# Kernel optimization log

Hardware: AMD Instinct MI355X
Metric: run time of the kernel (lower is better)

Reference implementation:

```python
import jax, jax.numpy as jnp
import numpy as np

B, S, HID = 1, 2048, 4096
NH, NKV, HD = 32, 8, 128
EPS = 1e-6
SCALE = HD ** -0.5


def _rope_cos_sin(seq_len, head_dim, base=1000000.0):
    inv_freq = 1.0 / (base ** (np.arange(0, head_dim, 2, dtype=np.float32) / head_dim))
    t = np.arange(seq_len, dtype=np.float32)
    freqs = np.outer(t, inv_freq)                      # [S, HD/2]
    emb = np.concatenate([freqs, freqs], axis=-1)       # [S, HD]
    return jnp.asarray(np.cos(emb))[None], jnp.asarray(np.sin(emb))[None]  # [1,S,HD]


def setup_inputs() -> dict:
    key = jax.random.key(0)
    ks = jax.random.split(key, 8)
    cos, sin = _rope_cos_sin(S, HD)
    inp = {
        "hidden_states": jax.random.normal(ks[0], (B, S, HID), jnp.float32),
        "cos": jnp.broadcast_to(cos, (B, S, HD)),
        "sin": jnp.broadcast_to(sin, (B, S, HD)),
        "Wq": jax.random.normal(ks[1], (NH * HD, HID), jnp.float32) * 0.02,
        "Wk": jax.random.normal(ks[2], (NKV * HD, HID), jnp.float32) * 0.02,
        "Wv": jax.random.normal(ks[3], (NKV * HD, HID), jnp.float32) * 0.02,
        "Wo": jax.random.normal(ks[4], (HID, NH * HD), jnp.float32) * 0.02,
        "q_norm_w": jnp.ones((HD,), jnp.float32),
        "k_norm_w": jnp.ones((HD,), jnp.float32),
    }
    return inp


def _rmsnorm(x, w, eps=EPS):
    var = jnp.mean(jnp.square(x), axis=-1, keepdims=True)
    return x * jax.lax.rsqrt(var + eps) * w


def _rotate_half(x):
    x1, x2 = jnp.split(x, 2, axis=-1)
    return jnp.concatenate([-x2, x1], axis=-1)


def _apply_rope(x, cos, sin):
    # x: [b,s,n,d]; cos/sin: [b,s,d] -> unsqueeze head dim (dim=2)
    c = cos[:, :, None, :]
    s = sin[:, :, None, :]
    return x * c + _rotate_half(x) * s


def reference(hidden_states, cos, sin, Wq, Wk, Wv, Wo, q_norm_w, k_norm_w):
    b, s, _ = hidden_states.shape
    q = (hidden_states @ Wq.T).reshape(b, s, NH, HD)
    k = (hidden_states @ Wk.T).reshape(b, s, NKV, HD)
    v = (hidden_states @ Wv.T).reshape(b, s, NKV, HD)
    # per-head RMSNorm on q and k
    q = _rmsnorm(q, q_norm_w)
    k = _rmsnorm(k, k_norm_w)
    # RoPE
    q = _apply_rope(q, cos, sin)
    k = _apply_rope(k, cos, sin)
    # GQA: expand kv heads to match query heads (group size = NH // NKV)
    g = NH // NKV
    k = jnp.repeat(k, g, axis=2)  # [b,s,NH,d]
    v = jnp.repeat(v, g, axis=2)
    # causal SDPA, layout bsnd
    scores = jnp.einsum("bqhd,bkhd->bhqk", q, k) * SCALE
    causal = jnp.tril(jnp.ones((s, s), dtype=bool))
    scores = jnp.where(causal[None, None], scores, jnp.finfo(scores.dtype).min)
    probs = jax.nn.softmax(scores, axis=-1)
    attn = jnp.einsum("bhqk,bkhd->bqhd", probs, v).reshape(b, s, NH * HD)
    return attn @ Wo.T
```

## Files before the change

kernel.cpp:

```cpp
#include <hip/hip_runtime.h>
#include <hip/hip_bf16.h>
#include <stdint.h>

#define S_LEN 2048
#define HIDD  4096
#define NH    32
#define NKV   8
#define HD    128
#define NQKV  6144
#define ATT_SCALE 0.08838834764831845f
#define LOG2E 1.4426950408889634f

typedef unsigned short u16;
typedef __attribute__((ext_vector_type(8))) short short8;
typedef __attribute__((ext_vector_type(4))) float f32x4;

__device__ __forceinline__ unsigned f2bfbits(float f){
  union{float f; unsigned u;} v; v.f = f;
  return (v.u + 0x7FFFu + ((v.u>>16)&1u)) >> 16;
}
__device__ __forceinline__ float bf2f(u16 b){
  union{unsigned u; float f;} v; v.u = ((unsigned)b)<<16;
  return v.f;
}
__device__ __forceinline__ unsigned packbf(float a, float b){
  return f2bfbits(a) | (f2bfbits(b)<<16);
}
__device__ __forceinline__ unsigned cvtpk(float lo, float hi){
  unsigned r;
  asm("v_cvt_pk_bf16_f32 %0, %1, %2" : "=v"(r) : "v"(lo), "v"(hi));
  return r;
}

#define GLOAD16(g, l) __builtin_amdgcn_global_load_lds( \
    (__attribute__((address_space(1))) void*)(g), \
    (__attribute__((address_space(3))) void*)(l), 16, 0, 0)

#define VMWAIT(n) asm volatile("s_waitcnt vmcnt(" #n ")" ::: "memory")
#define SCHED0() __builtin_amdgcn_sched_barrier(0)

__global__ __launch_bounds__(256) void cvt_all(const float* __restrict__ hs,
                                               const float* __restrict__ Wq,
                                               const float* __restrict__ Wk,
                                               const float* __restrict__ Wv,
                                               u16* __restrict__ Xb,
                                               u16* __restrict__ WQKV){
  const float* src; u16* dst; int n8;
  switch (blockIdx.y){
    case 0: src = hs; dst = Xb;                        n8 = S_LEN*HIDD/8;    break;
    case 1: src = Wq; dst = WQKV;                      n8 = NH*HD*HIDD/8;    break;
    case 2: src = Wk; dst = WQKV + (size_t)NH*HD*HIDD; n8 = NKV*HD*HIDD/8;   break;
    default:src = Wv; dst = WQKV + (size_t)(NH+NKV)*HD*HIDD; n8 = NKV*HD*HIDD/8; break;
  }
  int i = blockIdx.x*256 + threadIdx.x;
  if (i >= n8) return;
  const float4* p = (const float4*)src;
  float4 a = p[2*i], b = p[2*i+1];
  union { unsigned u[4]; short8 s; } o;
  o.u[0] = packbf(a.x, a.y); o.u[1] = packbf(a.z, a.w);
  o.u[2] = packbf(b.x, b.y); o.u[3] = packbf(b.z, b.w);
  *(short8*)(dst + (size_t)i*8) = o.s;
}

__global__ __launch_bounds__(256) void cvt_bf16(const float* __restrict__ in,
                                                u16* __restrict__ out, int n8){
  int i = blockIdx.x*256 + threadIdx.x;
  if (i >= n8) return;
  const float4* p = (const float4*)in;
  float4 a = p[2*i], b = p[2*i+1];
  union { unsigned u[4]; short8 s; } o;
  o.u[0] = packbf(a.x, a.y); o.u[1] = packbf(a.z, a.w);
  o.u[2] = packbf(b.x, b.y); o.u[3] = packbf(b.z, b.w);
  *(short8*)(out + (size_t)i*8) = o.s;
}

template<int BM, int BN, typename OT>
__global__ __launch_bounds__(256) void gemm_4ph(const u16* __restrict__ A,
                                                const u16* __restrict__ B,
                                                OT* __restrict__ C,
                                                int N, int K, int nbx){
  constexpr int MREP = BM/32;
  constexpr int NF   = BN/32;
  constexpr int AL   = BM/64;
  constexpr int BL   = BN/64;
  constexpr int ASZ  = BM*64;
  constexpr int BSZ  = BN*64;
  __shared__ __align__(16) char lds[4*ASZ + 4*BSZ];

  const int tid = threadIdx.x;
  const int w = tid>>6, lane = tid&63, ln = lane&15, g = lane>>4;
  const int wm = w>>1, wn = w&1;
  const int swz5 = ((ln>>3)&1)<<5;

  const int nwg = gridDim.x, flat = blockIdx.x;
  const int wg = (flat&7)*(nwg>>3) + (flat>>3);
  const int by = wg/nbx, bx = wg - by*nbx;
  const int m0 = by*BM, n0 = bx*BN;

  const int rs   = ((tid>>6)<<4) + ((tid&63)>>2);
  const int ksrc = ((tid&3)<<3) ^ (((tid>>5)&1)<<4);
  const u16* srcA[AL];
  #pragma unroll
  for (int j=0;j<AL;j++) srcA[j] = A + (size_t)(m0 + 64*j + rs)*K + ksrc;
  const u16* srcB[BL];
  #pragma unroll
  for (int j=0;j<BL;j++) srcB[j] = B + (size_t)(n0 + 64*j + rs)*K + ksrc;

  #define AREG(bf,kh) (lds + ((bf)*2 + (kh))*ASZ)
  #define BREG(bf,kh) (lds + 4*ASZ + ((bf)*2 + (kh))*BSZ)

  #define STAGEPT(t, kh, bf) { const int off_ = (t)*64 + (kh)*32;                 \
    _Pragma("unroll") for (int j=0;j<AL;j++)                                      \
      GLOAD16(srcA[j]+off_, AREG(bf,kh) + (4*j+w)*1024);                          \
    _Pragma("unroll") for (int j=0;j<BL;j++)                                      \
      GLOAD16(srcB[j]+off_, BREG(bf,kh) + (4*j+w)*1024); }

  f32x4 acc[MREP][NF];
  #pragma unroll
  for (int m=0;m<MREP;m++)
    #pragma unroll
    for (int n=0;n<NF;n++) acc[m][n] = (f32x4){0.f,0.f,0.f,0.f};
  short8 a_[MREP], b_[NF];

  #define READA(bf,kh) { _Pragma("unroll") for (int m=0;m<MREP;m++)               \
    a_[m] = *(const short8*)(AREG(bf,kh) + (wm*MREP+m)*1024 + ln*64 + ((g*16)^swz5)); }
  #define READB(bf,kh) { _Pragma("unroll") for (int n=0;n<NF;n++)                 \
    b_[n] = *(const short8*)(BREG(bf,kh) + (wn*NF+n)*1024 + ln*64 + ((g*16)^swz5)); }
  #define MFMACLU() { __builtin_amdgcn_s_setprio(1);                              \
    _Pragma("unroll") for (int m=0;m<MREP;m++)                                    \
      _Pragma("unroll") for (int n=0;n<NF;n++)                                    \
        acc[m][n] = __builtin_amdgcn_mfma_f32_16x16x32_bf16(a_[m], b_[n], acc[m][n], 0,0,0); \
    __builtin_amdgcn_s_setprio(0); }
  #define BARR() __builtin_amdgcn_s_barrier()
  #define VM2LP() do{ if constexpr (AL+BL==5) { VMWAIT(10); } else { VMWAIT(8); } }while(0)
  #define VM1LP() do{ if constexpr (AL+BL==5) { VMWAIT(5); }  else { VMWAIT(4); } }while(0)

  STAGEPT(0,0,0); STAGEPT(0,1,0); STAGEPT(1,0,1);
  VMWAIT(0); BARR(); SCHED0();

  const int NIT = K>>7;
  #pragma unroll 1
  for (int it=0; it<NIT; ++it){
    const bool last = (it == NIT-1);
    const int t0 = 2*it;
    READB(0,0); READA(0,0); STAGEPT(t0+1, 1, 1);
    MFMACLU();
    SCHED0(); VM2LP(); BARR(); SCHED0();
    READB(0,1); READA(0,1); if (!last) STAGEPT(t0+2, 0, 0);
    MFMACLU();
    SCHED0(); if (last) { VM1LP(); } else { VM2LP(); } BARR(); SCHED0();
    READB(1,0); READA(1,0); if (!last) STAGEPT(t0+2, 1, 0);
    MFMACLU();
    SCHED0(); if (last) { VMWAIT(0); } else { VM2LP(); } BARR(); SCHED0();
    READB(1,1); READA(1,1); if (!last) STAGEPT(t0+3, 0, 1);
    MFMACLU();
    SCHED0(); if (!last) { VM2LP(); } BARR(); SCHED0();
  }

  #pragma unroll
  for (int mi=0; mi<MREP; mi++)
    #pragma unroll
    for (int n=0; n<NF; n++)
      #pragma unroll
      for (int r=0;r<4;r++){
        int row = m0 + (wm*MREP+mi)*16 + g*4 + r;
        int col = n0 + (wn*NF+n)*16 + ln;
        if constexpr (__is_same(OT, u16))
          C[(size_t)row*N + col] = (u16)f2bfbits(acc[mi][n][r]);
        else
          C[(size_t)row*N + col] = acc[mi][n][r];
      }
  #undef AREG
  #undef BREG
  #undef STAGEPT
  #undef READA
  #undef READB
  #undef MFMACLU
  #undef BARR
  #undef VM2LP
  #undef VM1LP
}

__global__ __launch_bounds__(256) void norm_rope(const u16* __restrict__ QKVb,
                                                 const float* __restrict__ cosb,
                                                 const float* __restrict__ sinb,
                                                 const float* __restrict__ qw,
                                                 const float* __restrict__ kw,
                                                 u16* __restrict__ Qn,
                                                 u16* __restrict__ Kn,
                                                 u16* __restrict__ Vt){
  int w = threadIdx.x>>6, lane = threadIdx.x&63;
  int row = blockIdx.x*4 + w;
  int s = row / 48, slot = row - s*48;
  const u16* src = QKVb + (size_t)s*NQKV + slot*HD;
  float x0 = bf2f(src[lane]), x1 = bf2f(src[lane+64]);
  if (slot < 40){
    float ss = x0*x0 + x1*x1;
    #pragma unroll
    for (int off=1; off<64; off<<=1) ss += __shfl_xor(ss, off, 64);
    float r = rsqrtf(ss*(1.0f/128.0f) + 1e-6f);
    const float* wgt = (slot < 32) ? qw : kw;
    float y0 = x0*r*wgt[lane], y1 = x1*r*wgt[lane+64];
    float c0 = cosb[(size_t)s*HD+lane], c1 = cosb[(size_t)s*HD+lane+64];
    float s0 = sinb[(size_t)s*HD+lane], s1 = sinb[(size_t)s*HD+lane+64];
    float o0 = y0*c0 - y1*s0;
    float o1 = y1*c1 + y0*s1;
    float sc = (slot < 32) ? (ATT_SCALE*LOG2E) : 1.0f;
    u16* dst = (slot < 32) ? (Qn + ((size_t)slot*S_LEN + s)*HD)
                           : (Kn + ((size_t)(slot-32)*S_LEN + s)*HD);
    dst[lane]    = (u16)f2bfbits(o0*sc);
    dst[lane+64] = (u16)f2bfbits(o1*sc);
  } else {
    int kvh = slot - 40;
    u16* dst = Vt + (size_t)kvh*HD*S_LEN + s;
    dst[(size_t)lane*S_LEN]      = (u16)f2bfbits(x0);
    dst[(size_t)(lane+64)*S_LEN] = (u16)f2bfbits(x1);
  }
}

__global__ __launch_bounds__(256) void flash_attn(const u16* __restrict__ Qn,
                                                  const u16* __restrict__ Kn,
                                                  const u16* __restrict__ Vt,
                                                  u16* __restrict__ O){
  __shared__ u16 Ks[2][64*128];
  __shared__ u16 Vs[2][128*64];

  const int h = blockIdx.y;
  const int w = threadIdx.x>>6, lane = threadIdx.x&63, ln = lane&15, g = lane>>4;
  const int kvh = h>>2;
  const u16* Qh = Qn + (size_t)h*S_LEN*HD;
  const u16* Kh = Kn + (size_t)kvh*S_LEN*HD;
  const u16* Vh = Vt + (size_t)kvh*HD*S_LEN;

  const int krow_w = w*4 + g;
  const int ksw    = ((krow_w)&7)<<4;
  const int kcol   = ((ln*16) ^ ksw) >> 1;
  const int vrow_w = w*8 + (lane>>3);
  const int vsw    = ((lane>>3)&7)<<4;
  const int vcol   = (((lane&7)*16) ^ vsw) >> 1;

  #define STAGE_K(bufi, t) { \
    int kv0_ = (t)*64; \
    _Pragma("unroll") \
    for (int p=0;p<4;p++){ \
      const u16* ga = Kh + (size_t)(kv0_ + p*16 + krow_w)*HD + kcol; \
      GLOAD16(ga, (char*)&Ks[bufi][0] + p*4096 + w*1024); \
    } \
  }
  #define STAGE_V(bufi, t) { \
    int kv0_ = (t)*64; \
    _Pragma("unroll") \
    for (int p=0;p<4;p++){ \
      const u16* gv = Vh + (size_t)(p*32 + vrow_w)*S_LEN + kv0_ + vcol; \
      GLOAD16(gv, (char*)&Vs[bufi][0] + p*4096 + w*1024); \
    } \
  }
  #define QKT(dst, buf) { \
    _Pragma("unroll") for (int mt=0; mt<4; mt++){ \
      short8 kf[4]; \
      _Pragma("unroll") for (int c=0;c<4;c++) \
        kf[c] = *(const short8*)((const char*)&Ks[buf][0] \
                    + (mt*16+ln)*256 + ((c*64 + g*16) ^ ((ln&7)<<4))); \
      f32x4 qacc = (f32x4){0.f,0.f,0.f,0.f}; \
      __builtin_amdgcn_s_setprio(1); \
      _Pragma("unroll") for (int c=0;c<4;c++) \
        qacc = __builtin_amdgcn_mfma_f32_16x16x32_bf16(kf[c], qf[c], qacc, 0,0,0); \
      __builtin_amdgcn_s_setprio(0); \
      dst[mt] = qacc; \
    } }

  #define TILE_BODY(i, SC, SN) { \
    VMWAIT(0); \
    __builtin_amdgcn_s_barrier(); \
    if ((i)+1 < nt){ \
      QKT(SN, ((i)+1)&1); \
      if ((i)+2 < nt) STAGE_K(((i)+2)&1, (i)+2); \
      STAGE_V(((i)+1)&1, (i)+1); \
    } \
    const int kv0 = (i)*64; \
    float p[4][4]; \
    float mtile = -1e30f; \
    if ((i) < qb){ \
      _Pragma("unroll") for (int mt=0; mt<4; mt++) \
        _Pragma("unroll") for (int r=0;r<4;r++){ \
          p[mt][r] = SC[mt][r]; \
          mtile = fmaxf(mtile, SC[mt][r]); \
        } \
    } else { \
      _Pragma("unroll") for (int mt=0; mt<4; mt++) \
        _Pragma("unroll") for (int r=0;r<4;r++){ \
          int kv = kv0 + mt*16 + 4*g + r; \
          float sv = (kv <= qrow) ? SC[mt][r] : -1e30f; \
          p[mt][r] = sv; \
          mtile = fmaxf(mtile, sv); \
        } \
    } \
    mtile = fmaxf(mtile, __shfl_xor(mtile, 16, 64)); \
    mtile = fmaxf(mtile, __shfl_xor(mtile, 32, 64)); \
    bool defer = __all(mtile <= m_run + 11.5416f); \
    float m_new = defer ? m_run : fmaxf(m_run, mtile); \
    float l_tile = 0.f; \
    _Pragma("unroll") for (int mt=0; mt<4; mt++) \
      _Pragma("unroll") for (int r=0;r<4;r++){ \
        float e = exp2f(p[mt][r] - m_new); \
        p[mt][r] = e; \
        l_tile += e; \
      } \
    l_tile += __shfl_xor(l_tile, 16, 64); \
    l_tile += __shfl_xor(l_tile, 32, 64); \
    if (defer){ \
      l_run += l_tile; \
    } else { \
      float alpha = exp2f(m_run - m_new); \
      l_run = l_run*alpha + l_tile; \
      m_run = m_new; \
      _Pragma("unroll") for (int dt=0;dt<8;dt++) ot[dt] *= alpha; \
    } \
    short8 pf[2]; \
    _Pragma("unroll") for (int ks2=0; ks2<2; ks2++){ \
      unsigned pk00 = cvtpk(p[2*ks2  ][0], p[2*ks2  ][1]); \
      unsigned pk01 = cvtpk(p[2*ks2  ][2], p[2*ks2  ][3]); \
      unsigned pk10 = cvtpk(p[2*ks2+1][0], p[2*ks2+1][1]); \
      unsigned pk11 = cvtpk(p[2*ks2+1][2], p[2*ks2+1][3]); \
      int src0 = (((2*g  )&3)<<4) | ln; \
      int src1 = (((2*g+1)&3)<<4) | ln; \
      unsigned t00 = (unsigned)__shfl((int)pk00, src0, 64); \
      unsigned t10 = (unsigned)__shfl((int)pk10, src0, 64); \
      unsigned t01 = (unsigned)__shfl((int)pk01, src0, 64); \
      unsigned t11 = (unsigned)__shfl((int)pk11, src0, 64); \
      unsigned u00 = (unsigned)__shfl((int)pk00, src1, 64); \
      unsigned u10 = (unsigned)__shfl((int)pk10, src1, 64); \
      unsigned u01 = (unsigned)__shfl((int)pk01, src1, 64); \
      unsigned u11 = (unsigned)__shfl((int)pk11, src1, 64); \
      bool hiv = (g >= 2); \
      union { unsigned u[4]; short8 s; } pw; \
      pw.u[0] = hiv ? t10 : t00; \
      pw.u[1] = hiv ? t11 : t01; \
      pw.u[2] = hiv ? u10 : u00; \
      pw.u[3] = hiv ? u11 : u01; \
      pf[ks2] = pw.s; \
    } \
    _Pragma("unroll") for (int dt=0;dt<8;dt++){ \
      short8 vf[2]; \
      _Pragma("unroll") for (int ks2=0; ks2<2; ks2++) \
        vf[ks2] = *(const short8*)((const char*)&Vs[(i)&1][0] \
                    + (dt*16+ln)*128 + ((ks2*64 + g*16) ^ ((ln&7)<<4))); \
      __builtin_amdgcn_s_setprio(1); \
      _Pragma("unroll") for (int ks2=0; ks2<2; ks2++) \
        ot[dt] = __builtin_amdgcn_mfma_f32_16x16x32_bf16(vf[ks2], pf[ks2], ot[dt], 0,0,0); \
      __builtin_amdgcn_s_setprio(0); \
    } \
  }

  #pragma unroll 1
  for (int ph=0; ph<2; ph++){
    const int qb = ph ? (31 - blockIdx.x) : blockIdx.x;
    const int q0 = qb*64;
    const int qrow = q0 + w*16 + ln;

    short8 qf[4];
    #pragma unroll
    for (int c=0;c<4;c++)
      qf[c] = *(const short8*)(Qh + (size_t)qrow*HD + c*32 + g*8);

    f32x4 ot[8];
    #pragma unroll
    for (int dt=0;dt<8;dt++) ot[dt] = (f32x4){0.f,0.f,0.f,0.f};
    float m_run = -1e30f, l_run = 0.f;

    const int nt = qb + 1;

    STAGE_K(0, 0); STAGE_V(0, 0);
    if (nt > 1) STAGE_K(1, 1);
    VMWAIT(0);
    __builtin_amdgcn_s_barrier();

    f32x4 stA[4], stB[4];
    QKT(stA, 0);

    #pragma unroll 1
    for (int i=0; i<nt; i+=2){
      TILE_BODY(i, stA, stB);
      if (i+1 < nt) TILE_BODY(i+1, stB, stA);
    }
    __syncthreads();

    float inv = 1.0f / l_run;
    u16* orow = O + (size_t)qrow*(NH*HD) + h*HD;
    #pragma unroll
    for (int dt=0;dt<8;dt++){
      #pragma unroll
      for (int rr=0; rr<4; rr+=2){
        unsigned pkd = cvtpk(ot[dt][rr]*inv, ot[dt][rr+1]*inv);
        *(unsigned*)(orow + dt*16 + g*4 + rr) = pkd;
      }
    }
  }
  #undef STAGE_K
  #undef STAGE_V
  #undef QKT
  #undef TILE_BODY
}

extern "C" void kernel_launch(void* const* d_in, const int* in_sizes, int n_in,
                              void* d_out, int out_size, void* d_ws, size_t ws_size,
                              hipStream_t stream){
  (void)in_sizes; (void)n_in; (void)out_size; (void)ws_size;
  const float* hs   = (const float*)d_in[0];
  const float* cosb = (const float*)d_in[1];
  const float* sinb = (const float*)d_in[2];
  const float* Wq   = (const float*)d_in[3];
  const float* Wk   = (const float*)d_in[4];
  const float* Wv   = (const float*)d_in[5];
  const float* Wo   = (const float*)d_in[6];
  const float* qw   = (const float*)d_in[7];
  const float* kw   = (const float*)d_in[8];
  float* out = (float*)d_out;

  char* ws = (char*)d_ws;
  u16*   Xb    = (u16*)  (ws);
  u16*   WQKV  = (u16*)  (ws + 16777216);
  u16*   QKVb  = (u16*)  (ws + 67108864);
  u16*   attnB = (u16*)  (ws + 94371840);
  u16*   Qn    = (u16*)  (ws + 117440512);
  u16*   Kn    = (u16*)  (ws + 134217728);
  u16*   Vt    = (u16*)  (ws + 138412032);
  u16*   Wob   = WQKV;

  cvt_all<<<dim3(8192, 4), 256, 0, stream>>>(hs, Wq, Wk, Wv, Xb, WQKV);
  gemm_4ph<128,192,u16><<<512, 256, 0, stream>>>(Xb, WQKV, QKVb, NQKV, HIDD, NQKV/192);
  norm_rope<<<(S_LEN*48)/4, 256, 0, stream>>>(QKVb, cosb, sinb, qw, kw, Qn, Kn, Vt);
  cvt_bf16<<<(HIDD*NH*HD/8)/256, 256, 0, stream>>>(Wo, Wob, HIDD*NH*HD/8);
  flash_attn<<<dim3(16, NH), 256, 0, stream>>>(Qn, Kn, Vt, attnB);
  gemm_4ph<128,128,float><<<512, 256, 0, stream>>>(attnB, Wob, out, HIDD, HIDD, HIDD/128);
}
```

Baseline: 374.7 us.

## Switch GEMMs to 256-wide 8-wave tiles with split-K output projection

```diff
diff --git a/kernel.cpp b/kernel.cpp
--- a/kernel.cpp
+++ b/kernel.cpp
@@ -74,111 +74,144 @@
   *(short8*)(out + (size_t)i*8) = o.s;
 }
 
-template<int BM, int BN, typename OT>
-__global__ __launch_bounds__(256) void gemm_4ph(const u16* __restrict__ A,
+__global__ __launch_bounds__(256) void reduce_add(const u16* __restrict__ P0,
+                                                  const u16* __restrict__ P1,
+                                                  float* __restrict__ out, int n8){
+  int i = blockIdx.x*256 + threadIdx.x;
+  if (i >= n8) return;
+  short8 a = *(const short8*)(P0 + (size_t)i*8);
+  short8 b = *(const short8*)(P1 + (size_t)i*8);
+  float4 o0, o1;
+  o0.x = bf2f((u16)a[0]) + bf2f((u16)b[0]);
+  o0.y = bf2f((u16)a[1]) + bf2f((u16)b[1]);
+  o0.z = bf2f((u16)a[2]) + bf2f((u16)b[2]);
+  o0.w = bf2f((u16)a[3]) + bf2f((u16)b[3]);
+  o1.x = bf2f((u16)a[4]) + bf2f((u16)b[4]);
+  o1.y = bf2f((u16)a[5]) + bf2f((u16)b[5]);
+  o1.z = bf2f((u16)a[6]) + bf2f((u16)b[6]);
+  o1.w = bf2f((u16)a[7]) + bf2f((u16)b[7]);
+  float4* po = (float4*)(out + (size_t)i*8);
+  po[0] = o0; po[1] = o1;
+}
+
+template<int BM, int BN, int KS, typename OT>
+__global__ __launch_bounds__(512) void gemm_8ph(const u16* __restrict__ A,
                                                 const u16* __restrict__ B,
-                                                OT* __restrict__ C,
-                                                int N, int K, int nbx){
-  constexpr int MREP = BM/32;
-  constexpr int NF   = BN/32;
-  constexpr int AL   = BM/64;
-  constexpr int BL   = BN/64;
-  constexpr int ASZ  = BM*64;
-  constexpr int BSZ  = BN*64;
+                                                OT* __restrict__ C0,
+                                                OT* __restrict__ C1,
+                                                int N, int Kstride, int nbx){
+  constexpr int NF  = BN/64;
+  constexpr int ASZ = 16384;
+  constexpr int BSZ = 16384;
   __shared__ __align__(16) char lds[4*ASZ + 4*BSZ];
 
   const int tid = threadIdx.x;
   const int w = tid>>6, lane = tid&63, ln = lane&15, g = lane>>4;
-  const int wm = w>>1, wn = w&1;
+  const int wm = w>>2, wn = w&3;
   const int swz5 = ((ln>>3)&1)<<5;
 
   const int nwg = gridDim.x, flat = blockIdx.x;
   const int wg = (flat&7)*(nwg>>3) + (flat>>3);
-  const int by = wg/nbx, bx = wg - by*nbx;
+  const int ntile = nwg / KS;
+  const int ks = wg / ntile;
+  const int tb = wg - ks*ntile;
+  const int by = tb/nbx, bx = tb - by*nbx;
   const int m0 = by*BM, n0 = bx*BN;
+  const int Kext = Kstride / KS;
+  const size_t koff = (size_t)ks * Kext;
 
   const int rs   = ((tid>>6)<<4) + ((tid&63)>>2);
   const int ksrc = ((tid&3)<<3) ^ (((tid>>5)&1)<<4);
-  const u16* srcA[AL];
+  const u16* srcA[2];
   #pragma unroll
-  for (int j=0;j<AL;j++) srcA[j] = A + (size_t)(m0 + 64*j + rs)*K + ksrc;
-  const u16* srcB[BL];
+  for (int h=0;h<2;h++) srcA[h] = A + (size_t)(m0 + h*128 + rs)*Kstride + koff + ksrc;
+  const u16* srcB[2];
   #pragma unroll
-  for (int j=0;j<BL;j++) srcB[j] = B + (size_t)(n0 + 64*j + rs)*K + ksrc;
+  for (int h=0;h<2;h++) srcB[h] = B + (size_t)(n0 + h*128 + rs)*Kstride + koff + ksrc;
 
   #define AREG(bf,kh) (lds + ((bf)*2 + (kh))*ASZ)
   #define BREG(bf,kh) (lds + 4*ASZ + ((bf)*2 + (kh))*BSZ)
 
-  #define STAGEPT(t, kh, bf) { const int off_ = (t)*64 + (kh)*32;                 \
-    _Pragma("unroll") for (int j=0;j<AL;j++)                                      \
-      GLOAD16(srcA[j]+off_, AREG(bf,kh) + (4*j+w)*1024);                          \
-    _Pragma("unroll") for (int j=0;j<BL;j++)                                      \
-      GLOAD16(srcB[j]+off_, BREG(bf,kh) + (4*j+w)*1024); }
-
-  f32x4 acc[MREP][NF];
+  #define STAGE_A(t, kh, bf) { const int off_ = (t)*64 + (kh)*32;                 \
+    GLOAD16(srcA[0]+off_, AREG(bf,kh) + w*1024);                                  \
+    GLOAD16(srcA[1]+off_, AREG(bf,kh) + 8192 + w*1024); }
+  #define STAGE_B(t, kh, bf) { const int off_ = (t)*64 + (kh)*32;                 \
+    GLOAD16(srcB[0]+off_, BREG(bf,kh) + w*1024);                                  \
+    GLOAD16(srcB[1]+off_, BREG(bf,kh) + 8192 + w*1024); }
+
+  f32x4 acc[8][NF];
   #pragma unroll
-  for (int m=0;m<MREP;m++)
+  for (int m=0;m<8;m++)
     #pragma unroll
     for (int n=0;n<NF;n++) acc[m][n] = (f32x4){0.f,0.f,0.f,0.f};
-  short8 a_[MREP], b_[NF];
-
-  #define READA(bf,kh) { _Pragma("unroll") for (int m=0;m<MREP;m++)               \
-    a_[m] = *(const short8*)(AREG(bf,kh) + (wm*MREP+m)*1024 + ln*64 + ((g*16)^swz5)); }
+  short8 a_[4], b_[NF];
+
+  #define READA(bf,kh,mh) { _Pragma("unroll") for (int m=0;m<4;m++)               \
+    a_[m] = *(const short8*)(AREG(bf,kh) + (wm*8+(mh)*4+m)*1024 + ln*64 + ((g*16)^swz5)); }
   #define READB(bf,kh) { _Pragma("unroll") for (int n=0;n<NF;n++)                 \
     b_[n] = *(const short8*)(BREG(bf,kh) + (wn*NF+n)*1024 + ln*64 + ((g*16)^swz5)); }
-  #define MFMACLU() { __builtin_amdgcn_s_setprio(1);                              \
-    _Pragma("unroll") for (int m=0;m<MREP;m++)                                    \
+  #define MFMA16(mh) { __builtin_amdgcn_s_setprio(1);                             \
+    _Pragma("unroll") for (int m=0;m<4;m++)                                       \
       _Pragma("unroll") for (int n=0;n<NF;n++)                                    \
-        acc[m][n] = __builtin_amdgcn_mfma_f32_16x16x32_bf16(a_[m], b_[n], acc[m][n], 0,0,0); \
+        acc[(mh)*4+m][n] = __builtin_amdgcn_mfma_f32_16x16x32_bf16(a_[m], b_[n], acc[(mh)*4+m][n], 0,0,0); \
     __builtin_amdgcn_s_setprio(0); }
   #define BARR() __builtin_amdgcn_s_barrier()
-  #define VM2LP() do{ if constexpr (AL+BL==5) { VMWAIT(10); } else { VMWAIT(8); } }while(0)
-  #define VM1LP() do{ if constexpr (AL+BL==5) { VMWAIT(5); }  else { VMWAIT(4); } }while(0)
-
-  STAGEPT(0,0,0); STAGEPT(0,1,0); STAGEPT(1,0,1);
-  VMWAIT(0); BARR(); SCHED0();
-
-  const int NIT = K>>7;
+  #define LGK0() do{ asm volatile("s_waitcnt lgkmcnt(0)" ::: "memory"); SCHED0(); }while(0)
+
+  const int NT = Kext>>6;
+
+  STAGE_A(0,0,0); STAGE_B(0,0,0); STAGE_A(0,1,0); STAGE_B(0,1,0);
+  STAGE_A(1,0,1); STAGE_B(1,0,1);
+  VMWAIT(4); BARR(); SCHED0();
+
+  #define TILE4(bf, T) {                                                          \
+    const bool s1 = (T)+1 < NT, s2 = (T)+2 < NT;                                  \
+                                                \
+    READB(bf,0); READA(bf,0,0); if (s1) STAGE_A((T)+1, 1, bf^1);                  \
+    BARR(); LGK0(); MFMA16(0); BARR();                                            \
+                                                \
+    READA(bf,0,1); if (s1) STAGE_B((T)+1, 1, bf^1);                               \
+    BARR(); LGK0(); MFMA16(1); BARR();                                            \
+                        \
+    READB(bf,1); READA(bf,1,0); if (s2) STAGE_A((T)+2, 0, bf);                    \
+    BARR(); LGK0(); MFMA16(0); BARR();                                            \
+              \
+    READA(bf,1,1); if (s2) STAGE_B((T)+2, 0, bf);                                 \
+    BARR(); LGK0(); MFMA16(1);                                                    \
+    if ((T) >= NT-2) { VMWAIT(0); } else { VMWAIT(4); }                           \
+    BARR();                                                                       \
+  }
+
   #pragma unroll 1
-  for (int it=0; it<NIT; ++it){
-    const bool last = (it == NIT-1);
-    const int t0 = 2*it;
-    READB(0,0); READA(0,0); STAGEPT(t0+1, 1, 1);
-    MFMACLU();
-    SCHED0(); VM2LP(); BARR(); SCHED0();
-    READB(0,1); READA(0,1); if (!last) STAGEPT(t0+2, 0, 0);
-    MFMACLU();
-    SCHED0(); if (last) { VM1LP(); } else { VM2LP(); } BARR(); SCHED0();
-    READB(1,0); READA(1,0); if (!last) STAGEPT(t0+2, 1, 0);
-    MFMACLU();
-    SCHED0(); if (last) { VMWAIT(0); } else { VM2LP(); } BARR(); SCHED0();
-    READB(1,1); READA(1,1); if (!last) STAGEPT(t0+3, 0, 1);
-    MFMACLU();
-    SCHED0(); if (!last) { VM2LP(); } BARR(); SCHED0();
-  }
-
+  for (int T=0; T<NT; T+=2){
+    TILE4(0, T);
+    TILE4(1, T+1);
+  }
+
+  OT* Cw = (KS == 2 && ks == 1) ? C1 : C0;
   #pragma unroll
-  for (int mi=0; mi<MREP; mi++)
+  for (int mi=0; mi<8; mi++)
     #pragma unroll
     for (int n=0; n<NF; n++)
       #pragma unroll
       for (int r=0;r<4;r++){
-        int row = m0 + (wm*MREP+mi)*16 + g*4 + r;
-        int col = n0 + (wn*NF+n)*16 + ln;
+        int row = m0 + wm*128 + mi*16 + g*4 + r;
+        int col = n0 + wn*(NF*16) + n*16 + ln;
         if constexpr (__is_same(OT, u16))
-          C[(size_t)row*N + col] = (u16)f2bfbits(acc[mi][n][r]);
+          Cw[(size_t)row*N + col] = (u16)f2bfbits(acc[mi][n][r]);
         else
-          C[(size_t)row*N + col] = acc[mi][n][r];
+          Cw[(size_t)row*N + col] = acc[mi][n][r];
       }
   #undef AREG
   #undef BREG
-  #undef STAGEPT
+  #undef STAGE_A
+  #undef STAGE_B
   #undef READA
   #undef READB
-  #undef MFMACLU
+  #undef MFMA16
   #undef BARR
-  #undef VM2LP
-  #undef VM1LP
+  #undef LGK0
+  #undef TILE4
 }
 
 __global__ __launch_bounds__(256) void norm_rope(const u16* __restrict__ QKVb,
@@ -426,11 +459,14 @@
   u16*   Kn    = (u16*)  (ws + 134217728);
   u16*   Vt    = (u16*)  (ws + 138412032);
   u16*   Wob   = WQKV;
+  u16*   P0    = Xb;
+  u16*   P1    = QKVb;
 
   cvt_all<<<dim3(8192, 4), 256, 0, stream>>>(hs, Wq, Wk, Wv, Xb, WQKV);
-  gemm_4ph<128,192,u16><<<512, 256, 0, stream>>>(Xb, WQKV, QKVb, NQKV, HIDD, NQKV/192);
+  gemm_8ph<256,192,1,u16><<<256, 512, 0, stream>>>(Xb, WQKV, QKVb, nullptr, NQKV, HIDD, NQKV/192);
   norm_rope<<<(S_LEN*48)/4, 256, 0, stream>>>(QKVb, cosb, sinb, qw, kw, Qn, Kn, Vt);
   cvt_bf16<<<(HIDD*NH*HD/8)/256, 256, 0, stream>>>(Wo, Wob, HIDD*NH*HD/8);
   flash_attn<<<dim3(16, NH), 256, 0, stream>>>(Qn, Kn, Vt, attnB);
-  gemm_4ph<128,128,float><<<512, 256, 0, stream>>>(attnB, Wob, out, HIDD, HIDD, HIDD/128);
-}
+  gemm_8ph<256,256,2,u16><<<256, 512, 0, stream>>>(attnB, Wob, P0, P1, HIDD, HIDD, HIDD/256);
+  reduce_add<<<(S_LEN*HIDD/8)/256, 256, 0, stream>>>(P0, P1, out, S_LEN*HIDD/8);
+}
```

New measurement: 332.7 us. 1.13x faster.
